# Performance work log

Hardware: AMD Instinct MI355X
Metric: run time of the kernel (lower is better)

The kernel has to match this reference:

```python
import jax, jax.numpy as jnp
import numpy as np

MIN_NORM = 1e-15
BALL_EPS = 4e-3  # HGCN PoincareBall fp32 boundary eps
C = 1.0          # curvature (init kwarg c)
CLAMP = 1e6      # torch.clamp bound in HypAgg.forward


def _artanh(x):
    # torch Artanh clamps input into open (-1, 1); use fp32-safe eps
    return jnp.arctanh(jnp.clip(x, -1.0 + 1e-7, 1.0 - 1e-7))


def _norm(x):
    return jnp.maximum(jnp.linalg.norm(x, axis=-1, keepdims=True), MIN_NORM)


def mobius_add(x, y, c):
    x2 = jnp.sum(x * x, axis=-1, keepdims=True)
    y2 = jnp.sum(y * y, axis=-1, keepdims=True)
    xy = jnp.sum(x * y, axis=-1, keepdims=True)
    num = (1.0 + 2.0 * c * xy + c * y2) * x + (1.0 - c * x2) * y
    den = 1.0 + 2.0 * c * xy + (c * c) * x2 * y2
    return num / jnp.maximum(den, MIN_NORM)


def lambda_x(x, c):
    return 2.0 / jnp.maximum(1.0 - c * jnp.sum(x * x, axis=-1, keepdims=True), MIN_NORM)


def logmap(p1, p2, c):
    # log_{p1}(p2) on the Poincare ball
    sub = mobius_add(-p1, p2, c)
    sub_norm = _norm(sub)
    sqrt_c = c ** 0.5
    return (2.0 / sqrt_c / lambda_x(p1, c)) * _artanh(sqrt_c * sub_norm) * sub / sub_norm


def expmap(u, p, c):
    sqrt_c = c ** 0.5
    u_norm = _norm(u)
    second = jnp.tanh(sqrt_c / 2.0 * lambda_x(p, c) * u_norm) * u / (sqrt_c * u_norm)
    return mobius_add(p, second, c)


def proj(x, c):
    norm = _norm(x)
    maxnorm = (1.0 - BALL_EPS) / (c ** 0.5)
    return jnp.where(norm > maxnorm, x / norm * maxnorm, x)


def setup_inputs() -> dict:
    key = jax.random.key(0)
    kx, ka, kw = jax.random.split(key, 3)
    B, N, D = 2, 768, 64
    # points strictly inside the unit ball
    x = proj(0.2 * jax.random.normal(kx, (B, N, D), dtype=jnp.float32), C)
    adj = (jax.random.uniform(ka, (B, N, N), dtype=jnp.float32) < 0.05).astype(jnp.float32)
    att_W = jax.random.normal(kw, (2 * D, 1), dtype=jnp.float32) * (1.0 / np.sqrt(2 * D))
    att_b = jnp.zeros((1,), dtype=jnp.float32)
    return {"x": x, "adj": adj, "att_W": att_W, "att_b": att_b}


def reference(x, adj, att_W, att_b):
    c = C
    b, n, d = x.shape
    # pairwise tangent vectors: x_local[b,i,j] = log_{x_i}(x_j)   (b,n,n,d)
    x_i = x[:, :, None, :]
    x_j = x[:, None, :, :]
    x_local = logmap(x_i, x_j, c)
    # log_x(x) == 0 tangent, kept for faithfulness
    x_self = logmap(x, x, c)  # (b,n,d), ~0
    # DenseAtt: linear(2d->1) on [self_tangent || pairwise_tangent], sigmoid, masked by adj
    feats = jnp.concatenate(
        [jnp.broadcast_to(x_self[:, :, None, :], x_local.shape), x_local], axis=-1
    )  # (b,n,n,2d)
    logits = jnp.einsum('bijk,ko->bijo', feats, att_W)[..., 0] + att_b[0]  # (b,n,n)
    att = jax.nn.sigmoid(logits) * adj
    # attention-weighted tangent aggregation over neighbors j
    support_t = jnp.einsum('bij,bijd->bid', att, x_local)
    # proj_tan is identity on the Poincare ball
    support_t = jnp.clip(support_t, -CLAMP, CLAMP)
    return proj(expmap(support_t, x, c), c)
```

## Files before the change

### kernel.cpp

```cpp
#include <hip/hip_runtime.h>
#include <math.h>

#define NB 2
#define NN 768
#define ND 64

__device__ __forceinline__ float fmul_(float a, float b) { float r = a * b; asm volatile("" : "+v"(r)); return r; }
__device__ __forceinline__ float fadd_(float a, float b) { float r = a + b; asm volatile("" : "+v"(r)); return r; }

template <typename F>
__device__ __forceinline__ float pw64(F f) {
  float r[8];
#pragma unroll
  for (int m = 0; m < 8; ++m) r[m] = f(m);
#pragma unroll
  for (int i = 1; i < 8; ++i) {
#pragma unroll
    for (int m = 0; m < 8; ++m) r[m] = fadd_(r[m], f(8 * i + m));
  }
  const float s01 = fadd_(r[0], r[1]), s23 = fadd_(r[2], r[3]);
  const float s45 = fadd_(r[4], r[5]), s67 = fadd_(r[6], r[7]);
  return fadd_(fadd_(s01, s23), fadd_(s45, s67));
}

__device__ __forceinline__ float div_rn(float n, float d, float r) {
  const float q0 = n * r;
  const float e  = __builtin_fmaf(-d, q0, n);
  return __builtin_fmaf(e, r, q0);
}

__global__ __launch_bounds__(64) void k_main(const float* __restrict__ x,
                                             const float* __restrict__ adj,
                                             const float* __restrict__ attW,
                                             const float* __restrict__ attb,
                                             float* __restrict__ out) {
  __shared__ float xi_s[ND];
  __shared__ float sW2[ND];
  __shared__ float eb[ND];
  __shared__ int   lj[NN];
  __shared__ float lcf[NN];

  const int row  = blockIdx.x;
  const int b    = row / NN;
  const int lane = threadIdx.x;

  xi_s[lane] = x[(size_t)row * ND + lane];
  sW2[lane]  = attW[ND + lane];
  __syncthreads();

  eb[lane] = fmul_(xi_s[lane], xi_s[lane]);
  __syncthreads();
  const float ni = pw64([&](int k) { return eb[k]; });

  const float b1  = 1.0f - ni;
  const float lam = 2.0f / fmaxf(b1, 1e-15f);
  const float g1  = 2.0f / lam;
  const float ab  = attb[0];
  const float ATH_CLIP = (float)(1.0 - 1e-07);

  int count = 0;
  const float* __restrict__ arow = adj + (size_t)row * NN;
#pragma unroll
  for (int c = 0; c < NN / 64; ++c) {
    const int j = c * 64 + lane;
    const float aj = arow[j];
    const unsigned long long m = __ballot(aj != 0.0f);
    if (aj != 0.0f) {
      const int rank = __popcll(m & ((1ull << lane) - 1ull));
      lj[count + rank] = j;
    }
    count += __popcll(m);
  }
  __syncthreads();

  const float* __restrict__ xb = x + (size_t)b * NN * ND;
  float pP = 0.0f;
  for (int p = lane; p < count; p += 64) {
    const int j = lj[p];
    float rj[ND];
    const float4* __restrict__ xj4 = (const float4*)(xb + (size_t)j * ND);
#pragma unroll
    for (int k4 = 0; k4 < 16; ++k4) {
      const float4 v = xj4[k4];
      rj[4 * k4 + 0] = v.x; rj[4 * k4 + 1] = v.y;
      rj[4 * k4 + 2] = v.z; rj[4 * k4 + 3] = v.w;
    }
    const float nj = pw64([&](int k) { return fmul_(rj[k], rj[k]); });
    const float d  = pw64([&](int k) { return fmul_(xi_s[k], rj[k]); });
    const float xy = -d;
    const float t1  = fadd_(1.0f, 2.0f * xy);
    const float a1  = fadd_(t1, nj);
    const float den = fadd_(t1, fmul_(ni, nj));
    const float denc = fmaxf(den, 1e-15f);
    const float rden = 1.0f / denc;
    float racc[8];
    float subW = 0.0f;
#pragma unroll
    for (int m = 0; m < 8; ++m) {
      const float nk = fadd_(-fmul_(a1, xi_s[m]), fmul_(b1, rj[m]));
      const float sk = div_rn(nk, denc, rden);
      subW = __builtin_fmaf(sk, sW2[m], subW);
      racc[m] = fmul_(sk, sk);
    }
#pragma unroll
    for (int i8 = 1; i8 < 8; ++i8) {
#pragma unroll
      for (int m = 0; m < 8; ++m) {
        const int k = 8 * i8 + m;
        const float nk = fadd_(-fmul_(a1, xi_s[k]), fmul_(b1, rj[k]));
        const float sk = div_rn(nk, denc, rden);
        subW = __builtin_fmaf(sk, sW2[k], subW);
        racc[m] = fadd_(racc[m], fmul_(sk, sk));
      }
    }
    const float s01 = fadd_(racc[0], racc[1]), s23 = fadd_(racc[2], racc[3]);
    const float s45 = fadd_(racc[4], racc[5]), s67 = fadd_(racc[6], racc[7]);
    const float s2  = fadd_(fadd_(s01, s23), fadd_(s45, s67));
    const float t   = sqrtf(s2);
    const float sn  = fmaxf(t, 1e-15f);
    const float z   = fminf(sn, ATH_CLIP);
    const float ath = atanhf(z);
    const float g2  = fmul_(g1, ath);
    const float gg  = g2 / sn;
    const float logit = gg * subW + ab;
    const float sig   = 1.0f / (1.0f + expf(-logit));
    const float cfac  = sig * gg * rden;
    lcf[p] = cfac;
    pP = __builtin_fmaf(cfac, a1, pP);
  }
  float pw = pP;
#pragma unroll
  for (int m = 32; m >= 1; m >>= 1) pw += __shfl_xor(pw, m, 64);
  const float P = pw;
  __syncthreads();

  float Q0 = 0.0f, Q1 = 0.0f, Q2 = 0.0f, Q3 = 0.0f;
  for (int p = 0; p < count; ++p) {
    const int j  = lj[p];
    const float cf = lcf[p];
    const float v  = xb[(size_t)j * ND + lane];
    if (j < 192)      Q0 = __builtin_fmaf(cf, v, Q0);
    else if (j < 384) Q1 = __builtin_fmaf(cf, v, Q1);
    else if (j < 576) Q2 = __builtin_fmaf(cf, v, Q2);
    else              Q3 = __builtin_fmaf(cf, v, Q3);
  }
  const float Q = (Q0 + Q1) + (Q2 + Q3);

  const float xid = xi_s[lane];
  float u = b1 * Q - P * xid;
  u = fminf(fmaxf(u, -1e6f), 1e6f);
  __syncthreads();
  eb[lane] = fmul_(u, u);
  __syncthreads();
  const float u2 = pw64([&](int k) { return eb[k]; });
  const float un = fmaxf(sqrtf(u2), 1e-15f);
  const float th = tanhf(fmul_(0.5f * lam, un));
  const float sec = fmul_(th, u) / un;
  __syncthreads();
  eb[lane] = fmul_(sec, sec);
  __syncthreads();
  const float y2 = pw64([&](int k) { return eb[k]; });
  __syncthreads();
  eb[lane] = fmul_(xid, sec);
  __syncthreads();
  const float xys = pw64([&](int k) { return eb[k]; });
  const float t1e  = fadd_(1.0f, 2.0f * xys);
  const float a1e  = fadd_(t1e, y2);
  const float dene = fmaxf(fadd_(t1e, fmul_(ni, y2)), 1e-15f);
  const float o    = fadd_(fmul_(a1e, xid), fmul_(b1, sec)) / dene;
  __syncthreads();
  eb[lane] = fmul_(o, o);
  __syncthreads();
  const float o2 = pw64([&](int k) { return eb[k]; });
  const float nm = fmaxf(sqrtf(o2), 1e-15f);
  const float res = (nm > 0.996f) ? fmul_(o / nm, 0.996f) : o;
  out[(size_t)row * ND + lane] = res;
}

extern "C" void kernel_launch(void* const* d_in, const int* in_sizes, int n_in,
                              void* d_out, int out_size, void* d_ws, size_t ws_size,
                              hipStream_t stream) {
  const float* x    = (const float*)d_in[0];
  const float* adj  = (const float*)d_in[1];
  const float* attW = (const float*)d_in[2];
  const float* attb = (const float*)d_in[3];
  float* out = (float*)d_out;

  hipLaunchKernelGGL(k_main, dim3(NB * NN), dim3(64), 0, stream,
                     x, adj, attW, attb, out);
}
```

Before: 90.66 us.

## Stage neighbor rows in LDS and fuse aggregation into chunked pair loop

The pairwise loop now runs in chunks of 64 neighbors. Each lane writes its loaded neighbor row into a padded LDS tile, and the weighted aggregation reads those rows from LDS instead of reloading them from global memory in a separate pass. The adjacency row is also prefetched into registers before the first barrier, and neighbor indices are stored as shorts. This removes the second global gather over neighbor rows. In exchange it uses about 17KB of LDS per block, which may limit occupancy, and adds two barriers per chunk.

```diff
diff --git a/kernel.cpp b/kernel.cpp
--- a/kernel.cpp
+++ b/kernel.cpp
@@ -4,6 +4,7 @@
 #define NB 2
 #define NN 768
 #define ND 64
+#define XSTRIDE 68
 
 __device__ __forceinline__ float fmul_(float a, float b) { float r = a * b; asm volatile("" : "+v"(r)); return r; }
 __device__ __forceinline__ float fadd_(float a, float b) { float r = a + b; asm volatile("" : "+v"(r)); return r; }
@@ -37,8 +38,9 @@
   __shared__ float xi_s[ND];
   __shared__ float sW2[ND];
   __shared__ float eb[ND];
-  __shared__ int   lj[NN];
-  __shared__ float lcf[NN];
+  __shared__ short lj[NN];
+  __shared__ float lcf_s[64];
+  __shared__ float lds_x[64 * XSTRIDE];
 
   const int row  = blockIdx.x;
   const int b    = row / NN;
@@ -46,6 +48,12 @@
 
   xi_s[lane] = x[(size_t)row * ND + lane];
   sW2[lane]  = attW[ND + lane];
+
+  const float* __restrict__ arow = adj + (size_t)row * NN;
+  float av[NN / 64];
+#pragma unroll
+  for (int c = 0; c < NN / 64; ++c) av[c] = arow[c * 64 + lane];
+
   __syncthreads();
 
   eb[lane] = fmul_(xi_s[lane], xi_s[lane]);
@@ -59,15 +67,12 @@
   const float ATH_CLIP = (float)(1.0 - 1e-07);
 
   int count = 0;
-  const float* __restrict__ arow = adj + (size_t)row * NN;
 #pragma unroll
   for (int c = 0; c < NN / 64; ++c) {
-    const int j = c * 64 + lane;
-    const float aj = arow[j];
-    const unsigned long long m = __ballot(aj != 0.0f);
-    if (aj != 0.0f) {
+    const unsigned long long m = __ballot(av[c] != 0.0f);
+    if (av[c] != 0.0f) {
       const int rank = __popcll(m & ((1ull << lane) - 1ull));
-      lj[count + rank] = j;
+      lj[count + rank] = (short)(c * 64 + lane);
     }
     count += __popcll(m);
   }
@@ -75,75 +80,89 @@
 
   const float* __restrict__ xb = x + (size_t)b * NN * ND;
   float pP = 0.0f;
-  for (int p = lane; p < count; p += 64) {
-    const int j = lj[p];
-    float rj[ND];
-    const float4* __restrict__ xj4 = (const float4*)(xb + (size_t)j * ND);
-#pragma unroll
-    for (int k4 = 0; k4 < 16; ++k4) {
-      const float4 v = xj4[k4];
-      rj[4 * k4 + 0] = v.x; rj[4 * k4 + 1] = v.y;
-      rj[4 * k4 + 2] = v.z; rj[4 * k4 + 3] = v.w;
+  float Q0 = 0.0f, Q1 = 0.0f, Q2 = 0.0f, Q3 = 0.0f;
+
+  for (int base = 0; base < count; base += 64) {
+    const int valid = min(count - base, 64);
+
+    if (lane < valid) {
+      const int j = lj[base + lane];
+      float rj[ND];
+      const float4* __restrict__ xj4 = (const float4*)(xb + (size_t)j * ND);
+#pragma unroll
+      for (int k4 = 0; k4 < 16; ++k4) {
+        const float4 v = xj4[k4];
+        rj[4 * k4 + 0] = v.x; rj[4 * k4 + 1] = v.y;
+        rj[4 * k4 + 2] = v.z; rj[4 * k4 + 3] = v.w;
+      }
+      {
+        float4* __restrict__ dst = (float4*)&lds_x[lane * XSTRIDE];
+#pragma unroll
+        for (int k4 = 0; k4 < 16; ++k4)
+          dst[k4] = make_float4(rj[4 * k4], rj[4 * k4 + 1],
+                                rj[4 * k4 + 2], rj[4 * k4 + 3]);
+      }
+      const float nj = pw64([&](int k) { return fmul_(rj[k], rj[k]); });
+      const float d  = pw64([&](int k) { return fmul_(xi_s[k], rj[k]); });
+      const float xy = -d;
+      const float t1  = fadd_(1.0f, 2.0f * xy);
+      const float a1  = fadd_(t1, nj);
+      const float den = fadd_(t1, fmul_(ni, nj));
+      const float denc = fmaxf(den, 1e-15f);
+      const float rden = 1.0f / denc;
+      float racc[8];
+      float subW = 0.0f;
+#pragma unroll
+      for (int m = 0; m < 8; ++m) {
+        const float nk = fadd_(-fmul_(a1, xi_s[m]), fmul_(b1, rj[m]));
+        const float sk = div_rn(nk, denc, rden);
+        subW = __builtin_fmaf(sk, sW2[m], subW);
+        racc[m] = fmul_(sk, sk);
+      }
+#pragma unroll
+      for (int i8 = 1; i8 < 8; ++i8) {
+#pragma unroll
+        for (int m = 0; m < 8; ++m) {
+          const int k = 8 * i8 + m;
+          const float nk = fadd_(-fmul_(a1, xi_s[k]), fmul_(b1, rj[k]));
+          const float sk = div_rn(nk, denc, rden);
+          subW = __builtin_fmaf(sk, sW2[k], subW);
+          racc[m] = fadd_(racc[m], fmul_(sk, sk));
+        }
+      }
+      const float s01 = fadd_(racc[0], racc[1]), s23 = fadd_(racc[2], racc[3]);
+      const float s45 = fadd_(racc[4], racc[5]), s67 = fadd_(racc[6], racc[7]);
+      const float s2  = fadd_(fadd_(s01, s23), fadd_(s45, s67));
+      const float t   = sqrtf(s2);
+      const float sn  = fmaxf(t, 1e-15f);
+      const float z   = fminf(sn, ATH_CLIP);
+      const float ath = atanhf(z);
+      const float g2  = fmul_(g1, ath);
+      const float gg  = g2 / sn;
+      const float logit = gg * subW + ab;
+      const float sig   = 1.0f / (1.0f + expf(-logit));
+      const float cfac  = sig * gg * rden;
+      lcf_s[lane] = cfac;
+      pP = __builtin_fmaf(cfac, a1, pP);
     }
-    const float nj = pw64([&](int k) { return fmul_(rj[k], rj[k]); });
-    const float d  = pw64([&](int k) { return fmul_(xi_s[k], rj[k]); });
-    const float xy = -d;
-    const float t1  = fadd_(1.0f, 2.0f * xy);
-    const float a1  = fadd_(t1, nj);
-    const float den = fadd_(t1, fmul_(ni, nj));
-    const float denc = fmaxf(den, 1e-15f);
-    const float rden = 1.0f / denc;
-    float racc[8];
-    float subW = 0.0f;
-#pragma unroll
-    for (int m = 0; m < 8; ++m) {
-      const float nk = fadd_(-fmul_(a1, xi_s[m]), fmul_(b1, rj[m]));
-      const float sk = div_rn(nk, denc, rden);
-      subW = __builtin_fmaf(sk, sW2[m], subW);
-      racc[m] = fmul_(sk, sk);
+    __syncthreads();
+
+    for (int p2 = 0; p2 < valid; ++p2) {
+      const int   j  = lj[base + p2];
+      const float cf = lcf_s[p2];
+      const float v  = lds_x[p2 * XSTRIDE + lane];
+      if (j < 192)      Q0 = __builtin_fmaf(cf, v, Q0);
+      else if (j < 384) Q1 = __builtin_fmaf(cf, v, Q1);
+      else if (j < 576) Q2 = __builtin_fmaf(cf, v, Q2);
+      else              Q3 = __builtin_fmaf(cf, v, Q3);
     }
-#pragma unroll
-    for (int i8 = 1; i8 < 8; ++i8) {
-#pragma unroll
-      for (int m = 0; m < 8; ++m) {
-        const int k = 8 * i8 + m;
-        const float nk = fadd_(-fmul_(a1, xi_s[k]), fmul_(b1, rj[k]));
-        const float sk = div_rn(nk, denc, rden);
-        subW = __builtin_fmaf(sk, sW2[k], subW);
-        racc[m] = fadd_(racc[m], fmul_(sk, sk));
-      }
-    }
-    const float s01 = fadd_(racc[0], racc[1]), s23 = fadd_(racc[2], racc[3]);
-    const float s45 = fadd_(racc[4], racc[5]), s67 = fadd_(racc[6], racc[7]);
-    const float s2  = fadd_(fadd_(s01, s23), fadd_(s45, s67));
-    const float t   = sqrtf(s2);
-    const float sn  = fmaxf(t, 1e-15f);
-    const float z   = fminf(sn, ATH_CLIP);
-    const float ath = atanhf(z);
-    const float g2  = fmul_(g1, ath);
-    const float gg  = g2 / sn;
-    const float logit = gg * subW + ab;
-    const float sig   = 1.0f / (1.0f + expf(-logit));
-    const float cfac  = sig * gg * rden;
-    lcf[p] = cfac;
-    pP = __builtin_fmaf(cfac, a1, pP);
+    __syncthreads();
   }
+
   float pw = pP;
 #pragma unroll
   for (int m = 32; m >= 1; m >>= 1) pw += __shfl_xor(pw, m, 64);
   const float P = pw;
-  __syncthreads();
-
-  float Q0 = 0.0f, Q1 = 0.0f, Q2 = 0.0f, Q3 = 0.0f;
-  for (int p = 0; p < count; ++p) {
-    const int j  = lj[p];
-    const float cf = lcf[p];
-    const float v  = xb[(size_t)j * ND + lane];
-    if (j < 192)      Q0 = __builtin_fmaf(cf, v, Q0);
-    else if (j < 384) Q1 = __builtin_fmaf(cf, v, Q1);
-    else if (j < 576) Q2 = __builtin_fmaf(cf, v, Q2);
-    else              Q3 = __builtin_fmaf(cf, v, Q3);
-  }
   const float Q = (Q0 + Q1) + (Q2 + Q3);
 
   const float xid = xi_s[lane];
```

Result: faster. 85.08 us (-6.2%).
